# Optimization experiments

Hardware: AMD Instinct MI355X
Metric: run time of the kernel (lower is better)

Reference implementation:

```python
import jax, jax.numpy as jnp
import numpy as np

# dims
B_, L_, DM = 2, 2048, 2048
DS, DC, EXP, HD, NG, CH = 128, 4, 2, 64, 1, 256
DI = EXP * DM                    # d_inner = d_ssm = 4096
NH = DI // HD                    # 64 heads
DIP = 2 * DI + 2 * NG * DS + NH  # 8448 in_proj output
CDIM = DI + 2 * NG * DS          # 4352 conv channels
EPS = 1e-5


def setup_inputs() -> dict:
    key = jax.random.key(0)
    ks = jax.random.split(key, 6)
    u = jax.random.normal(ks[0], (B_, L_, DM), jnp.float32)
    w_in = jax.random.normal(ks[1], (DM, DIP), jnp.float32) * 0.02
    conv_w = jax.random.normal(ks[2], (CDIM, DC), jnp.float32) * (1.0 / np.sqrt(DC))
    conv_b = jnp.zeros((CDIM,), jnp.float32)
    # dt_bias init exactly as the torch module (dt_min=1e-3, dt_max=0.1)
    dt = jnp.exp(jax.random.uniform(ks[3], (NH,)) * (np.log(0.1) - np.log(0.001)) + np.log(0.001))
    dt = jnp.clip(dt, 1e-4)
    dt_bias = dt + jnp.log(-jnp.expm1(-dt))
    A_log = jnp.log(jax.random.uniform(ks[4], (NH,), minval=1.0, maxval=16.0))
    D_skip = jnp.ones((NH,), jnp.float32)
    norm_w = jnp.ones((DI,), jnp.float32)
    return dict(u=u, w_in=w_in, conv_w=conv_w, conv_b=conv_b,
                dt_bias=dt_bias, A_log=A_log, D_skip=D_skip, norm_w=norm_w)


def _segsum(x):
    # x: (..., T) -> (..., T, T) lower-triangular segment sums, -inf above diag
    T = x.shape[-1]
    cs = jnp.cumsum(x, -1)
    ss = cs[..., :, None] - cs[..., None, :]
    return jnp.where(jnp.tril(jnp.ones((T, T), bool)), ss, -jnp.inf)


def _ssd(xdt, dA, Bm, Cm):
    # xdt: (b,l,h,p) = x*dt, dA: (b,l,h) = dt*A, Bm/Cm: (b,l,g,n)
    b, l, h, p = xdt.shape
    c = l // CH
    xr = xdt.reshape(b, c, CH, h, p)
    dAr = dA.reshape(b, c, CH, h).transpose(0, 3, 1, 2)        # (b,h,c,t)
    rep = h // NG
    Bh = jnp.repeat(Bm.reshape(b, c, CH, NG, DS), rep, axis=3)  # (b,c,t,h,n)
    Ch = jnp.repeat(Cm.reshape(b, c, CH, NG, DS), rep, axis=3)
    Acs = jnp.cumsum(dAr, -1)                                   # (b,h,c,t)
    Lm = jnp.exp(_segsum(dAr))                                  # (b,h,c,t,t)
    # intra-chunk (diagonal block) output
    Yd = jnp.einsum('bcthn,bcshn,bhcts,bcshp->bcthp', Ch, Bh, Lm, xr)
    # per-chunk final states
    decay_st = jnp.exp(Acs[..., -1:] - Acs)                     # (b,h,c,t)
    states = jnp.einsum('bcthn,bhct,bcthp->bchpn', Bh, decay_st, xr)
    # inter-chunk recurrence
    pad_last = jnp.pad(Acs[..., -1], ((0, 0), (0, 0), (1, 0)))  # (b,h,c+1)
    dchunk = jnp.exp(_segsum(pad_last))                         # (b,h,c+1,c+1)
    states = jnp.concatenate([jnp.zeros_like(states[:, :1]), states], 1)
    init_st = jnp.einsum('bhzc,bchpn->bzhpn', dchunk, states)[:, :-1]  # (b,c,h,p,n)
    Yo = jnp.einsum('bcthn,bchpn,bhct->bcthp', Ch, init_st, jnp.exp(Acs))
    return (Yd + Yo).reshape(b, l, h, p)


def reference(u, w_in, conv_w, conv_b, dt_bias, A_log, D_skip, norm_w):
    zxbcdt = u @ w_in                           # (b,l,8448)
    z = zxbcdt[..., :DI]
    xBC = zxbcdt[..., DI:DI + CDIM]
    dt = zxbcdt[..., DI + CDIM:]                # (b,l,nheads)
    # causal depthwise conv1d (kernel DC, left pad DC-1) + SiLU
    xp = jnp.pad(xBC, ((0, 0), (DC - 1, 0), (0, 0)))
    xBC = sum(xp[:, k:k + L_, :] * conv_w[:, k] for k in range(DC)) + conv_b
    xBC = jax.nn.silu(xBC)
    x = xBC[..., :DI].reshape(B_, L_, NH, HD)
    Bm = xBC[..., DI:DI + NG * DS].reshape(B_, L_, NG, DS)
    Cm = xBC[..., DI + NG * DS:].reshape(B_, L_, NG, DS)
    dt = jax.nn.softplus(dt + dt_bias)          # dt_softplus=True
    A = -jnp.exp(A_log)
    y = _ssd(x * dt[..., None], dt * A, Bm, Cm)
    y = y + x * D_skip[None, None, :, None]     # D skip, per-head
    y = y.reshape(B_, L_, DI)
    # gated RMSNorm, norm_before_gate=False: rmsnorm(y * silu(z)) * weight
    yg = y * jax.nn.silu(z)
    return yg * jax.lax.rsqrt(jnp.mean(yg * yg, -1, keepdims=True) + EPS) * norm_w
```

## Files before the change

kernel.cpp:

```cpp
#include <hip/hip_runtime.h>
#include <hip/hip_bf16.h>

#define B_SZ   2
#define L_SZ   2048
#define DM     2048
#define DS     128
#define DCV    4
#define HD     64
#define CH     256
#define DI     4096
#define NH     64
#define DIP    8512
#define CDIM   4352
#define NP     8576
#define MROWS  4096
#define NCK    8

typedef __attribute__((ext_vector_type(8))) short bf16x8;
typedef __attribute__((ext_vector_type(4))) float f32x4;
typedef unsigned short u16;

__device__ __forceinline__ u16 f2bf(float f) {
    union { float f; unsigned u; } c; c.f = f;
    unsigned r = c.u + 0x7fffu + ((c.u >> 16) & 1u);
    return (u16)(r >> 16);
}
__device__ __forceinline__ float bf2f(u16 b) {
    union { unsigned u; float f; } c; c.u = ((unsigned)b) << 16; return c.f;
}

__device__ __forceinline__ void async16(const u16* g, u16* l) {
    __builtin_amdgcn_global_load_lds(
        (const __attribute__((address_space(1))) unsigned int*)(g),
        (__attribute__((address_space(3))) unsigned int*)(l),
        16, 0, 0);
}

__global__ void cvt_u_kernel(const float* __restrict__ u, u16* __restrict__ ub) {
    int i = blockIdx.x * 256 + threadIdx.x;
    float4 v = ((const float4*)u)[i];
    ushort4 o;
    o.x = f2bf(v.x); o.y = f2bf(v.y); o.z = f2bf(v.z); o.w = f2bf(v.w);
    ((ushort4*)ub)[i] = o;
}

__global__ void transpose_w_kernel(const float* __restrict__ w, u16* __restrict__ wt) {
    __shared__ float tile[32][33];
    int n0 = blockIdx.x * 32, k0 = blockIdx.y * 32;
    int tx = threadIdx.x & 31, ty = threadIdx.x >> 5;
    for (int j = 0; j < 32; j += 8) {
        int k = k0 + ty + j, n = n0 + tx;
        tile[ty + j][tx] = (n < DIP) ? w[(size_t)k * DIP + n] : 0.f;
    }
    __syncthreads();
    for (int j = 0; j < 32; j += 8) {
        int n = n0 + ty + j, k = k0 + tx;
        wt[(size_t)n * DM + k] = f2bf(tile[tx][ty + j]);
    }
}

#define GEMM_NM 32
#define GEMM_NN 67
#define GEMM_GM 8
__global__ __launch_bounds__(256) void gemm_kernel(const u16* __restrict__ A,
                                                   const u16* __restrict__ Bt,
                                                   u16* __restrict__ C) {
    __shared__ u16 As[128 * 64];
    __shared__ u16 Bs[128 * 64];
    const int bid = blockIdx.x;
    const int width = GEMM_GM * GEMM_NN;
    const int group = bid / width;
    const int rem = bid - group * width;
    const int pid_m = group * GEMM_GM + (rem % GEMM_GM);
    const int pid_n = rem / GEMM_GM;
    const int m0 = pid_m * 128, n0 = pid_n * 128;

    const int tid = threadIdx.x;
    const int lane = tid & 63, w = tid >> 6;
    const int wm = (w >> 1) * 64, wn = (w & 1) * 64;
    const int quad = lane >> 4, lm = lane & 15;
    const int lr = lane >> 3;
    const int pc = lane & 7;
    const int lcl = ((pc ^ lr) * 8);
    const int sx = (lm & 7);
    f32x4 acc[4][4] = {};
    for (int k0 = 0; k0 < DM; k0 += 64) {
        __syncthreads();
        for (int j = 0; j < 4; j++) {
            int row = w * 32 + j * 8 + lr;
            async16(A  + (size_t)(m0 + row) * DM + k0 + lcl, As + row * 64 + pc * 8);
            async16(Bt + (size_t)(n0 + row) * DM + k0 + lcl, Bs + row * 64 + pc * 8);
        }
        __syncthreads();
        for (int half = 0; half < 2; half++) {
            int cq = half * 4 + quad;
            int co = (cq ^ sx) * 8;
            bf16x8 af[4], bfr[4];
            for (int i = 0; i < 4; i++) af[i]  = *(const bf16x8*)(As + (wm + i * 16 + lm) * 64 + co);
            for (int j = 0; j < 4; j++) bfr[j] = *(const bf16x8*)(Bs + (wn + j * 16 + lm) * 64 + co);
            for (int i = 0; i < 4; i++)
                for (int j = 0; j < 4; j++)
                    acc[i][j] = __builtin_amdgcn_mfma_f32_16x16x32_bf16(af[i], bfr[j], acc[i][j], 0, 0, 0);
        }
    }
    for (int i = 0; i < 4; i++)
        for (int j = 0; j < 4; j++)
            for (int r = 0; r < 4; r++) {
                int gm = m0 + wm + i * 16 + quad * 4 + r;
                int gn = n0 + wn + j * 16 + lm;
                C[(size_t)gm * NP + gn] = f2bf(acc[i][j][r]);
            }
}

__global__ void conv_silu_kernel(const u16* __restrict__ zx, const float* __restrict__ cw,
                                 const float* __restrict__ cb, u16* __restrict__ xbc) {
    int c = blockIdx.x * 256 + threadIdx.x;
    int row = blockIdx.y;
    int l = row & (L_SZ - 1);
    float acc = cb[c];
    for (int k = 0; k < DCV; k++) {
        int ls = l - 3 + k;
        if (ls >= 0) acc += bf2f(zx[(size_t)(row - 3 + k) * NP + DI + c]) * cw[c * DCV + k];
    }
    float s = acc / (1.f + expf(-acc));
    xbc[(size_t)row * CDIM + c] = f2bf(s);
}

__global__ void dt_scan_kernel(const u16* __restrict__ zx, const float* __restrict__ dt_bias,
                               const float* __restrict__ A_log, float* __restrict__ dtbT,
                               float* __restrict__ acs) {
    int bid = blockIdx.x;
    int h = bid & 63, c = (bid >> 6) & 7, b = bid >> 9;
    int t = threadIdx.x;
    int row = b * L_SZ + c * CH + t;
    float raw = bf2f(zx[(size_t)row * NP + (DI + CDIM) + h]) + dt_bias[h];
    float dtv = (raw > 20.f) ? raw : log1pf(expf(raw));
    float dA = dtv * (-expf(A_log[h]));
    dtbT[(size_t)h * MROWS + row] = dtv;
    __shared__ float sc[256];
    sc[t] = dA;
    for (int off = 1; off < 256; off <<= 1) {
        __syncthreads();
        float v = (t >= off) ? sc[t - off] : 0.f;
        __syncthreads();
        sc[t] += v;
    }
    acs[((size_t)((b * NH + h) * NCK + c)) * CH + t] = sc[t];
}

__global__ void g_kernel(const u16* __restrict__ xbc, u16* __restrict__ Gb) {
    int blk = blockIdx.x;
    int bc = blk >> 4;
    int tile = blk & 15;
    int tb0 = (tile >> 2) * 64, sb0 = (tile & 3) * 64;
    int row0 = bc * CH;
    __shared__ float Ct[64][65], Bt_[64][65];
    int tq = (threadIdx.x >> 4) * 4;
    int sq = (threadIdx.x & 15) * 4;
    float acc[4][4] = {};
    for (int nh = 0; nh < 2; nh++) {
        __syncthreads();
        int r = threadIdx.x >> 2, cc = (threadIdx.x & 3) * 16;
        for (int q = 0; q < 16; q += 4) {
            ushort4 cv = *(const ushort4*)&xbc[(size_t)(row0 + tb0 + r) * CDIM + (DI + DS) + nh * 64 + cc + q];
            ushort4 bv = *(const ushort4*)&xbc[(size_t)(row0 + sb0 + r) * CDIM + DI + nh * 64 + cc + q];
            Ct[r][cc + q] = bf2f(cv.x); Ct[r][cc + q + 1] = bf2f(cv.y); Ct[r][cc + q + 2] = bf2f(cv.z); Ct[r][cc + q + 3] = bf2f(cv.w);
            Bt_[r][cc + q] = bf2f(bv.x); Bt_[r][cc + q + 1] = bf2f(bv.y); Bt_[r][cc + q + 2] = bf2f(bv.z); Bt_[r][cc + q + 3] = bf2f(bv.w);
        }
        __syncthreads();
        for (int n = 0; n < 64; n++) {
            float a[4], bb[4];
            for (int i = 0; i < 4; i++) a[i] = Ct[tq + i][n];
            for (int j = 0; j < 4; j++) bb[j] = Bt_[sq + j][n];
            for (int i = 0; i < 4; i++)
                for (int j = 0; j < 4; j++) acc[i][j] += a[i] * bb[j];
        }
    }
    for (int i = 0; i < 4; i++)
        for (int j = 0; j < 4; j++) {
            int t = tb0 + tq + i, s = sb0 + sq + j;
            Gb[((size_t)(bc * CH + t)) * CH + s] = (s <= t) ? f2bf(acc[i][j]) : (u16)0;
        }
}

__global__ void bmt_kernel(const u16* __restrict__ xbc, u16* __restrict__ BmT) {
    __shared__ u16 tile[64 * 72];
    int n0 = blockIdx.x * 64, r0 = blockIdx.y * 64;
    int tid = threadIdx.x;
    {
        int r = tid >> 2, seg = (tid & 3) * 16;
        const u16* src = xbc + (size_t)(r0 + r) * CDIM + DI + n0 + seg;
        *(int4*)(tile + r * 72 + seg)     = *(const int4*)(src);
        *(int4*)(tile + r * 72 + seg + 8) = *(const int4*)(src + 8);
    }
    __syncthreads();
    {
        int n = tid >> 2, seg = (tid & 3) * 16;
        union { u16 v[16]; int4 q[2]; } o;
        for (int q = 0; q < 16; q++) o.v[q] = tile[(seg + q) * 72 + n];
        u16* dst = BmT + (size_t)(n0 + n) * MROWS + r0 + seg;
        *(int4*)(dst)     = o.q[0];
        *(int4*)(dst + 8) = o.q[1];
    }
}

__global__ __launch_bounds__(256) void states_kernel(const u16* __restrict__ xbc, const u16* __restrict__ BmT,
                                                     const float* __restrict__ dtbT, const float* __restrict__ acs_g,
                                                     float* __restrict__ states) {
    int bid = blockIdx.x;
    int h = bid & 63, c = (bid >> 6) & 7, b = bid >> 9;
    int row0 = b * L_SZ + c * CH;
    int tid = threadIdx.x;
    int lane = tid & 63, w = tid >> 6;
    int quad = lane >> 4, lm = lane & 15;
    int mh = (w >> 1) * 32, nh = (w & 1) * 64;

    __shared__ float wsc[CH];
    __shared__ u16 XTs[64 * 136];

    {
        size_t abase = ((size_t)((b * NH + h) * NCK + c)) * CH;
        float a255 = acs_g[abase + 255];
        float at = acs_g[abase + tid];
        wsc[tid] = dtbT[(size_t)h * MROWS + row0 + tid] * expf(a255 - at);
    }
    f32x4 acc[2][4] = {};
    for (int k0 = 0; k0 < CH; k0 += 128) {
        __syncthreads();
        {
            int tl = tid >> 1;
            int pseg = (tid & 1) * 32;
            float wv = wsc[k0 + tl];
            const u16* xr = xbc + (size_t)(row0 + k0 + tl) * CDIM + h * HD + pseg;
            for (int q4 = 0; q4 < 4; q4++) {
                bf16x8 v = *(const bf16x8*)(xr + q4 * 8);
                for (int e = 0; e < 8; e++)
                    XTs[(pseg + q4 * 8 + e) * 136 + tl] = f2bf(bf2f((u16)v[e]) * wv);
            }
        }
        __syncthreads();
        for (int ks = 0; ks < 4; ks++) {
            bf16x8 af[2];
            for (int i = 0; i < 2; i++)
                af[i] = *(const bf16x8*)(XTs + (mh + i * 16 + lm) * 136 + ks * 32 + quad * 8);
            for (int j = 0; j < 4; j++) {
                const u16* brow = BmT + (size_t)(nh + j * 16 + lm) * MROWS + row0 + k0 + ks * 32 + quad * 8;
                bf16x8 bfr = *(const bf16x8*)brow;
                for (int i = 0; i < 2; i++)
                    acc[i][j] = __builtin_amdgcn_mfma_f32_16x16x32_bf16(af[i], bfr, acc[i][j], 0, 0, 0);
            }
        }
    }
    float* st = states + (size_t)bid * (HD * DS);
    for (int i = 0; i < 2; i++)
        for (int j = 0; j < 4; j++)
            for (int r = 0; r < 4; r++) {
                int p = mh + i * 16 + quad * 4 + r;
                int n = nh + j * 16 + lm;
                st[p * DS + n] = acc[i][j][r];
            }
}

__global__ void cscan_kernel(float* __restrict__ states, const float* __restrict__ acs_g) {
    int bid = blockIdx.x;
    int h = bid & 63, b = bid >> 6;
    int tid = threadIdx.x;
    float4 carry[8];
    for (int i = 0; i < 8; i++) carry[i] = make_float4(0.f, 0.f, 0.f, 0.f);
    for (int c = 0; c < NCK; c++) {
        size_t base = ((size_t)((b * NCK + c) * NH + h)) * (HD * DS);
        float g = expf(acs_g[((size_t)((b * NH + h) * NCK + c)) * CH + (CH - 1)]);
        float4* sp = (float4*)(states + base);
        for (int i = 0; i < 8; i++) {
            int idx = tid + 256 * i;
            float4 s = sp[idx];
            sp[idx] = carry[i];
            carry[i].x = carry[i].x * g + s.x;
            carry[i].y = carry[i].y * g + s.y;
            carry[i].z = carry[i].z * g + s.z;
            carry[i].w = carry[i].w * g + s.w;
        }
    }
}

__global__ __launch_bounds__(256) void y_kernel(const u16* __restrict__ xbc, const float* __restrict__ dtbT,
                                                const float* __restrict__ acs_g, const u16* __restrict__ Gb,
                                                const float* __restrict__ init_st, const float* __restrict__ D_skip,
                                                u16* __restrict__ y) {
    int bid = blockIdx.x;
    int h = bid & 63, c = (bid >> 6) & 7, b = bid >> 9;
    int bc = b * NCK + c;
    int row0 = b * L_SZ + c * CH;
    int tid = threadIdx.x;
    int lane = tid & 63, w = tid >> 6;
    int wt = w * 64;
    int quad = lane >> 4, lm = lane & 15;

    __shared__ float acs[CH];
    __shared__ u16 Ssb[64 * 136];
    __shared__ u16 XT[64 * 72];

    acs[tid] = acs_g[((size_t)((b * NH + h) * NCK + c)) * CH + tid];
    {
        const float4* sg = (const float4*)(init_st + ((size_t)(bc * NH + h)) * (HD * DS));
        for (int i = 0; i < 8; i++) {
            int g = tid + 256 * i;
            int p = g >> 5, n4 = (g & 31) * 4;
            float4 v = sg[g];
            ushort4 o;
            o.x = f2bf(v.x); o.y = f2bf(v.y); o.z = f2bf(v.z); o.w = f2bf(v.w);
            *(ushort4*)(Ssb + p * 136 + n4) = o;
        }
    }
    __syncthreads();

    f32x4 acc[4][4] = {};
    for (int i = 0; i < 4; i++) {
        const u16* arow = xbc + (size_t)(row0 + wt + i * 16 + lm) * CDIM + (DI + DS);
        for (int ks = 0; ks < 4; ks++) {
            bf16x8 af = *(const bf16x8*)(arow + ks * 32 + quad * 8);
            for (int j = 0; j < 4; j++) {
                bf16x8 bfr = *(const bf16x8*)(Ssb + (j * 16 + lm) * 136 + ks * 32 + quad * 8);
                acc[i][j] = __builtin_amdgcn_mfma_f32_16x16x32_bf16(af, bfr, acc[i][j], 0, 0, 0);
            }
        }
    }
    for (int i = 0; i < 4; i++) {
        float et[4];
        for (int r = 0; r < 4; r++) et[r] = expf(acs[wt + i * 16 + quad * 4 + r]);
        for (int j = 0; j < 4; j++)
            for (int r = 0; r < 4; r++) acc[i][j][r] *= et[r];
    }

    const u16* gball = Gb + (size_t)bc * CH * CH;
    for (int s0 = 0; s0 < CH; s0 += 64) {
        __syncthreads();
        {
            int r = tid >> 2, cseg = (tid & 3) * 16;
            int row = row0 + s0 + r;
            float dv = dtbT[(size_t)h * MROWS + row];
            const u16* xr = xbc + (size_t)row * CDIM + h * HD + cseg;
            for (int q8 = 0; q8 < 2; q8++) {
                bf16x8 v = *(const bf16x8*)(xr + q8 * 8);
                for (int e = 0; e < 8; e++)
                    XT[(cseg + q8 * 8 + e) * 72 + r] = f2bf(bf2f((u16)v[e]) * dv);
            }
        }
        __syncthreads();
        if (wt + 63 < s0) continue;
        for (int i = 0; i < 4; i++) {
            int tTop = wt + i * 16 + 15;
            if (tTop < s0) continue;
            int t = wt + i * 16 + lm;
            float at = acs[t];
            const u16* grow_ = gball + (size_t)t * CH + s0;
            for (int ks = 0; ks < 2; ks++) {
                if (s0 + ks * 32 > tTop) continue;
                bf16x8 g8 = *(const bf16x8*)(grow_ + ks * 32 + quad * 8);
                const float* asp = &acs[s0 + ks * 32 + quad * 8];
                bf16x8 af;
                for (int e = 0; e < 8; e++) {
                    float m = bf2f((u16)g8[e]) * expf(fminf(at - asp[e], 0.f));
                    af[e] = (short)f2bf(m);
                }
                for (int j = 0; j < 4; j++) {
                    bf16x8 bfr = *(const bf16x8*)(XT + (j * 16 + lm) * 72 + ks * 32 + quad * 8);
                    acc[i][j] = __builtin_amdgcn_mfma_f32_16x16x32_bf16(af, bfr, acc[i][j], 0, 0, 0);
                }
            }
        }
    }

    float dsk = D_skip[h];
    for (int i = 0; i < 4; i++)
        for (int r = 0; r < 4; r++) {
            int grow = row0 + wt + i * 16 + quad * 4 + r;
            const u16* xrow = xbc + (size_t)grow * CDIM + h * HD;
            u16* yrow = y + (size_t)grow * DI + h * HD;
            for (int j = 0; j < 4; j++) {
                int p = j * 16 + lm;
                yrow[p] = f2bf(acc[i][j][r] + dsk * bf2f(xrow[p]));
            }
        }
}

__global__ void final_kernel(const u16* __restrict__ y, const u16* __restrict__ zx,
                             const float* __restrict__ norm_w, float* __restrict__ out) {
    int row = blockIdx.x;
    int tid = threadIdx.x;
    __shared__ float red[4];
    float yg[16];
    float ss = 0.f;
    for (int i = 0; i < 16; i++) {
        int col = tid + 256 * i;
        float z = bf2f(zx[(size_t)row * NP + col]);
        float g = bf2f(y[(size_t)row * DI + col]) * (z / (1.f + expf(-z)));
        yg[i] = g; ss += g * g;
    }
    for (int off = 32; off; off >>= 1) ss += __shfl_down(ss, off);
    if ((tid & 63) == 0) red[tid >> 6] = ss;
    __syncthreads();
    if (tid == 0) red[0] = red[0] + red[1] + red[2] + red[3];
    __syncthreads();
    float inv = rsqrtf(red[0] / (float)DI + 1e-5f);
    for (int i = 0; i < 16; i++) {
        int col = tid + 256 * i;
        out[(size_t)row * DI + col] = yg[i] * inv * norm_w[col];
    }
}

extern "C" void kernel_launch(void* const* d_in, const int* in_sizes, int n_in,
                              void* d_out, int out_size, void* d_ws, size_t ws_size,
                              hipStream_t stream) {
    const float* u       = (const float*)d_in[0];
    const float* w_in    = (const float*)d_in[1];
    const float* conv_w  = (const float*)d_in[2];
    const float* conv_b  = (const float*)d_in[3];
    const float* dt_bias = (const float*)d_in[4];
    const float* A_log   = (const float*)d_in[5];
    const float* D_skip  = (const float*)d_in[6];
    const float* norm_w  = (const float*)d_in[7];
    float* out = (float*)d_out;

    const size_t NEEDED = 179306496ull;
    if (ws_size < NEEDED) return;

    char* ws = (char*)d_ws;
    const size_t R = 70254592ull;
    u16*   zx   = (u16*)ws;
    u16*   ubf  = (u16*)(ws + R);
    u16*   wtb  = (u16*)(ws + R + 16777216);
    u16*   xbc  = (u16*)(ws + R);
    float* dtbT = (float*)(ws + R + 35651584);
    float* acs  = (float*)(ws + R + 36700160);
    u16*   Gb   = (u16*)(ws + R + 37748736);
    u16*   BmT  = (u16*)(ws + R + 39845888);
    float* stat = (float*)(ws + R + 41943040);
    u16*   yb   = (u16*)(ws + R + 75497472);

    cvt_u_kernel<<<8192, 256, 0, stream>>>(u, ubf);
    transpose_w_kernel<<<dim3(268, 64), 256, 0, stream>>>(w_in, wtb);
    gemm_kernel<<<GEMM_NM * GEMM_NN, 256, 0, stream>>>(ubf, wtb, zx);
    conv_silu_kernel<<<dim3(17, 4096), 256, 0, stream>>>(zx, conv_w, conv_b, xbc);
    dt_scan_kernel<<<1024, 256, 0, stream>>>(zx, dt_bias, A_log, dtbT, acs);
    g_kernel<<<256, 256, 0, stream>>>(xbc, Gb);
    bmt_kernel<<<dim3(2, 64), 256, 0, stream>>>(xbc, BmT);
    states_kernel<<<1024, 256, 0, stream>>>(xbc, BmT, dtbT, acs, stat);
    cscan_kernel<<<128, 256, 0, stream>>>(stat, acs);
    y_kernel<<<1024, 256, 0, stream>>>(xbc, dtbT, acs, Gb, stat, D_skip, yb);
    final_kernel<<<4096, 256, 0, stream>>>(yb, zx, norm_w, out);
}
```

Measured before the change: 542.0 us.

## Rewrite in_proj GEMM with 256x128 tiles and triple-buffered async pipeline

The in_proj bf16 GEMM now uses 512-thread blocks computing 256x128 tiles. A three-stage LDS ring is prefetched with async global-to-LDS loads two k-tiles ahead, and each k-step is split into two MFMA phases interleaved with partial loads, explicit waitcnt, barriers and setprio. Block ids are also remapped across XCDs before the grouped tile ordering. This aims to hide global memory latency and raise MFMA utilisation, at the cost of 144KB of LDS per block (one block per CU) and fragile hand-tuned synchronisation.

After: 548.2 us. No clear change (+1.1%).

```diff
diff --git a/kernel.cpp b/kernel.cpp
--- a/kernel.cpp
+++ b/kernel.cpp
@@ -59,50 +59,106 @@
     }
 }
 
-#define GEMM_NM 32
-#define GEMM_NN 67
-#define GEMM_GM 8
-__global__ __launch_bounds__(256) void gemm_kernel(const u16* __restrict__ A,
+#define G_NKT   32
+#define G_NBLK  1072
+__global__ __launch_bounds__(512) void gemm_kernel(const u16* __restrict__ A,
                                                    const u16* __restrict__ Bt,
                                                    u16* __restrict__ C) {
-    __shared__ u16 As[128 * 64];
-    __shared__ u16 Bs[128 * 64];
-    const int bid = blockIdx.x;
-    const int width = GEMM_GM * GEMM_NN;
-    const int group = bid / width;
-    const int rem = bid - group * width;
-    const int pid_m = group * GEMM_GM + (rem % GEMM_GM);
-    const int pid_n = rem / GEMM_GM;
-    const int m0 = pid_m * 128, n0 = pid_n * 128;
+    __shared__ u16 As[3][256 * 64];
+    __shared__ u16 Bs[3][128 * 64];
+
+    int bid = blockIdx.x;
+    int bidx = (bid & 7) * (G_NBLK / 8) + (bid >> 3);
+    const int width = 8 * 67;
+    int group = bidx / width;
+    int rem = bidx - group * width;
+    int pid_m = group * 8 + (rem & 7);
+    int pid_n = rem >> 3;
+    const int m0 = pid_m * 256, n0 = pid_n * 128;
 
     const int tid = threadIdx.x;
-    const int lane = tid & 63, w = tid >> 6;
-    const int wm = (w >> 1) * 64, wn = (w & 1) * 64;
+    const int lane = tid & 63, wid = tid >> 6;
+    const int wm = (wid >> 1) * 64;
+    const int wn = (wid & 1) * 64;
     const int quad = lane >> 4, lm = lane & 15;
-    const int lr = lane >> 3;
-    const int pc = lane & 7;
-    const int lcl = ((pc ^ lr) * 8);
-    const int sx = (lm & 7);
+    const int sx = lm & 7;
+
+    const int srow = tid >> 3;
+    const int sc8 = (tid & 7) ^ (srow & 7);
+    const u16* aS = A  + (size_t)(m0 + srow) * DM + sc8 * 8;
+    const u16* bS = Bt + (size_t)(n0 + srow) * DM + sc8 * 8;
+    const int ldo = srow * 64 + (tid & 7) * 8;
+
     f32x4 acc[4][4] = {};
-    for (int k0 = 0; k0 < DM; k0 += 64) {
-        __syncthreads();
-        for (int j = 0; j < 4; j++) {
-            int row = w * 32 + j * 8 + lr;
-            async16(A  + (size_t)(m0 + row) * DM + k0 + lcl, As + row * 64 + pc * 8);
-            async16(Bt + (size_t)(n0 + row) * DM + k0 + lcl, Bs + row * 64 + pc * 8);
-        }
-        __syncthreads();
-        for (int half = 0; half < 2; half++) {
-            int cq = half * 4 + quad;
-            int co = (cq ^ sx) * 8;
-            bf16x8 af[4], bfr[4];
-            for (int i = 0; i < 4; i++) af[i]  = *(const bf16x8*)(As + (wm + i * 16 + lm) * 64 + co);
-            for (int j = 0; j < 4; j++) bfr[j] = *(const bf16x8*)(Bs + (wn + j * 16 + lm) * 64 + co);
+
+    for (int t = 0; t < 2; t++) {
+        const u16* as = aS + t * 64;
+        const u16* bs = bS + t * 64;
+        for (int q = 0; q < 4; q++) async16(as + (size_t)q * 64 * DM, &As[t][ldo + q * 4096]);
+        for (int q = 0; q < 2; q++) async16(bs + (size_t)q * 64 * DM, &Bs[t][ldo + q * 4096]);
+    }
+    asm volatile("s_waitcnt vmcnt(6)" ::: "memory");
+    __builtin_amdgcn_s_barrier();
+
+    for (int kt = 0; kt < G_NKT; kt++) {
+        unsigned cur = (unsigned)kt % 3u;
+        unsigned sb  = (unsigned)(kt + 2) % 3u;
+        const bool dost = (kt + 2) < G_NKT;
+        const u16* ab = &As[cur][0];
+        const u16* bb = &Bs[cur][0];
+        const u16* as = aS + (kt + 2) * 64;
+        const u16* bs = bS + (kt + 2) * 64;
+
+        bf16x8 af[4][2], bf0[2][2];
+        for (int i = 0; i < 4; i++) {
+            int row = wm + i * 16 + lm;
+            for (int ks = 0; ks < 2; ks++)
+                af[i][ks] = *(const bf16x8*)(ab + row * 64 + (((ks * 4 + quad) ^ sx) * 8));
+        }
+        for (int j = 0; j < 2; j++) {
+            int row = wn + j * 16 + lm;
+            for (int ks = 0; ks < 2; ks++)
+                bf0[j][ks] = *(const bf16x8*)(bb + row * 64 + (((ks * 4 + quad) ^ sx) * 8));
+        }
+        if (dost) {
+            async16(as,                   &As[sb][ldo]);
+            async16(as + (size_t)64 * DM, &As[sb][ldo + 4096]);
+            async16(bs,                   &Bs[sb][ldo]);
+        }
+        __builtin_amdgcn_s_barrier();
+        asm volatile("s_waitcnt lgkmcnt(0)" ::: "memory");
+        __builtin_amdgcn_s_setprio(1);
+        for (int ks = 0; ks < 2; ks++)
             for (int i = 0; i < 4; i++)
-                for (int j = 0; j < 4; j++)
-                    acc[i][j] = __builtin_amdgcn_mfma_f32_16x16x32_bf16(af[i], bfr[j], acc[i][j], 0, 0, 0);
-        }
-    }
+                for (int j = 0; j < 2; j++)
+                    acc[i][j] = __builtin_amdgcn_mfma_f32_16x16x32_bf16(af[i][ks], bf0[j][ks], acc[i][j], 0, 0, 0);
+        __builtin_amdgcn_s_setprio(0);
+        __builtin_amdgcn_s_barrier();
+
+        bf16x8 bf1[2][2];
+        for (int j = 0; j < 2; j++) {
+            int row = wn + (j + 2) * 16 + lm;
+            for (int ks = 0; ks < 2; ks++)
+                bf1[j][ks] = *(const bf16x8*)(bb + row * 64 + (((ks * 4 + quad) ^ sx) * 8));
+        }
+        if (dost) {
+            async16(as + (size_t)128 * DM, &As[sb][ldo + 8192]);
+            async16(as + (size_t)192 * DM, &As[sb][ldo + 12288]);
+            async16(bs + (size_t)64 * DM,  &Bs[sb][ldo + 4096]);
+        }
+        if (kt < G_NKT - 2) { asm volatile("s_waitcnt vmcnt(6)" ::: "memory"); }
+        else                { asm volatile("s_waitcnt vmcnt(0)" ::: "memory"); }
+        __builtin_amdgcn_s_barrier();
+        asm volatile("s_waitcnt lgkmcnt(0)" ::: "memory");
+        __builtin_amdgcn_s_setprio(1);
+        for (int ks = 0; ks < 2; ks++)
+            for (int i = 0; i < 4; i++)
+                for (int j = 0; j < 2; j++)
+                    acc[i][j + 2] = __builtin_amdgcn_mfma_f32_16x16x32_bf16(af[i][ks], bf1[j][ks], acc[i][j + 2], 0, 0, 0);
+        __builtin_amdgcn_s_setprio(0);
+        __builtin_amdgcn_s_barrier();
+    }
+
     for (int i = 0; i < 4; i++)
         for (int j = 0; j < 4; j++)
             for (int r = 0; r < 4; r++) {
@@ -440,7 +496,7 @@
 
     cvt_u_kernel<<<8192, 256, 0, stream>>>(u, ubf);
     transpose_w_kernel<<<dim3(268, 64), 256, 0, stream>>>(w_in, wtb);
-    gemm_kernel<<<GEMM_NM * GEMM_NN, 256, 0, stream>>>(ubf, wtb, zx);
+    gemm_kernel<<<G_NBLK, 512, 0, stream>>>(ubf, wtb, zx);
     conv_silu_kernel<<<dim3(17, 4096), 256, 0, stream>>>(zx, conv_w, conv_b, xbc);
     dt_scan_kernel<<<1024, 256, 0, stream>>>(zx, dt_bias, A_log, dtbT, acs);
     g_kernel<<<256, 256, 0, stream>>>(xbc, Gb);
```

## Vectorize conv and final-norm kernels and remap GEMM blocks across XCDs

Applied to the files above, without the earlier changes.

The conv+SiLU kernel now handles 8 channels per thread using 16-byte bf16 loads and stores. It uses a 512-thread block covering 16 rows, which cuts the launch from 69k blocks to about 4k. The final gated RMSNorm kernel loads z and y as bf16x8 vectors and writes float4 outputs, with each thread owning 16 contiguous columns. The GEMM remaps block IDs so that grouped tiles sharing A/B data land on the same XCD, improving L2 reuse. Contiguous per-thread columns can lower coalescing per instruction, but the wider accesses should cut the instruction count.

After: 532.8 us. No clear change (-1.7%).

```diff
diff --git a/kernel.cpp b/kernel.cpp
--- a/kernel.cpp
+++ b/kernel.cpp
@@ -67,7 +67,8 @@
                                                    u16* __restrict__ C) {
     __shared__ u16 As[128 * 64];
     __shared__ u16 Bs[128 * 64];
-    const int bid = blockIdx.x;
+    const int bid0 = blockIdx.x;
+    const int bid = (bid0 & 7) * ((GEMM_NM * GEMM_NN) / 8) + (bid0 >> 3);
     const int width = GEMM_GM * GEMM_NN;
     const int group = bid / width;
     const int rem = bid - group * width;
@@ -114,16 +115,41 @@
 
 __global__ void conv_silu_kernel(const u16* __restrict__ zx, const float* __restrict__ cw,
                                  const float* __restrict__ cb, u16* __restrict__ xbc) {
-    int c = blockIdx.x * 256 + threadIdx.x;
-    int row = blockIdx.y;
+    int tid = threadIdx.x;
+    int c8  = blockIdx.x * 32 + (tid & 31);
+    int row = blockIdx.y * 16 + (tid >> 5);
+    int c0  = c8 * 8;
     int l = row & (L_SZ - 1);
-    float acc = cb[c];
+
+    float w_[8][4];
+    {
+        const float4* wp = (const float4*)(cw + (size_t)c0 * 4);
+        for (int e = 0; e < 8; e++) {
+            float4 v = wp[e];
+            w_[e][0] = v.x; w_[e][1] = v.y; w_[e][2] = v.z; w_[e][3] = v.w;
+        }
+    }
+    float acc[8];
+    {
+        float4 b0 = *(const float4*)(cb + c0);
+        float4 b1 = *(const float4*)(cb + c0 + 4);
+        acc[0] = b0.x; acc[1] = b0.y; acc[2] = b0.z; acc[3] = b0.w;
+        acc[4] = b1.x; acc[5] = b1.y; acc[6] = b1.z; acc[7] = b1.w;
+    }
     for (int k = 0; k < DCV; k++) {
         int ls = l - 3 + k;
-        if (ls >= 0) acc += bf2f(zx[(size_t)(row - 3 + k) * NP + DI + c]) * cw[c * DCV + k];
-    }
-    float s = acc / (1.f + expf(-acc));
-    xbc[(size_t)row * CDIM + c] = f2bf(s);
+        if (ls >= 0) {
+            bf16x8 v = *(const bf16x8*)(zx + (size_t)(row - 3 + k) * NP + DI + c0);
+            for (int e = 0; e < 8; e++)
+                acc[e] += bf2f((u16)v[e]) * w_[e][k];
+        }
+    }
+    bf16x8 o;
+    for (int e = 0; e < 8; e++) {
+        float s = acc[e] / (1.f + expf(-acc[e]));
+        o[e] = (short)f2bf(s);
+    }
+    *(bf16x8*)(xbc + (size_t)row * CDIM + c0) = o;
 }
 
 __global__ void dt_scan_kernel(const u16* __restrict__ zx, const float* __restrict__ dt_bias,
@@ -388,14 +414,25 @@
                              const float* __restrict__ norm_w, float* __restrict__ out) {
     int row = blockIdx.x;
     int tid = threadIdx.x;
+    int col0 = tid * 16;
     __shared__ float red[4];
     float yg[16];
     float ss = 0.f;
-    for (int i = 0; i < 16; i++) {
-        int col = tid + 256 * i;
-        float z = bf2f(zx[(size_t)row * NP + col]);
-        float g = bf2f(y[(size_t)row * DI + col]) * (z / (1.f + expf(-z)));
-        yg[i] = g; ss += g * g;
+    {
+        bf16x8 zv0 = *(const bf16x8*)(zx + (size_t)row * NP + col0);
+        bf16x8 zv1 = *(const bf16x8*)(zx + (size_t)row * NP + col0 + 8);
+        bf16x8 yv0 = *(const bf16x8*)(y  + (size_t)row * DI + col0);
+        bf16x8 yv1 = *(const bf16x8*)(y  + (size_t)row * DI + col0 + 8);
+        for (int e = 0; e < 8; e++) {
+            float z = bf2f((u16)zv0[e]);
+            float g = bf2f((u16)yv0[e]) * (z / (1.f + expf(-z)));
+            yg[e] = g; ss += g * g;
+        }
+        for (int e = 0; e < 8; e++) {
+            float z = bf2f((u16)zv1[e]);
+            float g = bf2f((u16)yv1[e]) * (z / (1.f + expf(-z)));
+            yg[8 + e] = g; ss += g * g;
+        }
     }
     for (int off = 32; off; off >>= 1) ss += __shfl_down(ss, off);
     if ((tid & 63) == 0) red[tid >> 6] = ss;
@@ -403,9 +440,14 @@
     if (tid == 0) red[0] = red[0] + red[1] + red[2] + red[3];
     __syncthreads();
     float inv = rsqrtf(red[0] / (float)DI + 1e-5f);
-    for (int i = 0; i < 16; i++) {
-        int col = tid + 256 * i;
-        out[(size_t)row * DI + col] = yg[i] * inv * norm_w[col];
+    for (int q = 0; q < 4; q++) {
+        float4 nw = *(const float4*)(norm_w + col0 + q * 4);
+        float4 o;
+        o.x = yg[q * 4 + 0] * inv * nw.x;
+        o.y = yg[q * 4 + 1] * inv * nw.y;
+        o.z = yg[q * 4 + 2] * inv * nw.z;
+        o.w = yg[q * 4 + 3] * inv * nw.w;
+        *(float4*)(out + (size_t)row * DI + col0 + q * 4) = o;
     }
 }
 
@@ -441,7 +483,7 @@
     cvt_u_kernel<<<8192, 256, 0, stream>>>(u, ubf);
     transpose_w_kernel<<<dim3(268, 64), 256, 0, stream>>>(w_in, wtb);
     gemm_kernel<<<GEMM_NM * GEMM_NN, 256, 0, stream>>>(ubf, wtb, zx);
-    conv_silu_kernel<<<dim3(17, 4096), 256, 0, stream>>>(zx, conv_w, conv_b, xbc);
+    conv_silu_kernel<<<dim3(17, 256), 512, 0, stream>>>(zx, conv_w, conv_b, xbc);
     dt_scan_kernel<<<1024, 256, 0, stream>>>(zx, dt_bias, A_log, dtbT, acs);
     g_kernel<<<256, 256, 0, stream>>>(xbc, Gb);
     bmt_kernel<<<dim3(2, 64), 256, 0, stream>>>(xbc, BmT);
```
